# Kernel tuning notes

Measured on AMD Instinct MI355X. Metric: run time of the kernel, lower is better.

## Reference

```python
import jax, jax.numpy as jnp
import numpy as np

V, E, H, L = 32000, 512, 512, 2


def _cell(x, h, c, Wih, Whh, bih, bhh):
    # PyTorch LSTM cell, gate order i,f,g,o
    g = x @ Wih.T + bih + h @ Whh.T + bhh
    i, f, gg, o = jnp.split(g, 4, axis=-1)
    c = jax.nn.sigmoid(f) * c + jax.nn.sigmoid(i) * jnp.tanh(gg)
    h = jax.nn.sigmoid(o) * jnp.tanh(c)
    return h, c


def _run_layer(x, p):
    # x: [B, S, in], scan over time
    B = x.shape[0]
    h0 = jnp.zeros((B, H), x.dtype)

    def step(carry, xt):
        h, c = carry
        h, c = _cell(xt, h, c, *p)
        return (h, c), h

    (hT, cT), hs = jax.lax.scan(step, (h0, h0), jnp.swapaxes(x, 0, 1))
    return jnp.swapaxes(hs, 0, 1), hT, cT


def _forward(xs, ys, emb, enc_p, dec_p, attn_W, comb_W):
    # ---- Encoder (2-layer unidirectional LSTM) ----
    x = emb[xs]                      # [B, Senc, E]
    hs, cs = [], []
    for l in range(L):
        x, hT, cT = _run_layer(x, enc_p[l])
        hs.append(hT)
        cs.append(cT)
    enc_out = x                      # [B, Senc, H] (top layer)
    h = jnp.stack(hs)                # [L, B, H]
    c = jnp.stack(cs)
    neg = (1.0 - (xs > 0).astype(enc_out.dtype)) * 1e20  # [B, Senc]
    emb_out = jax.lax.stop_gradient(emb)  # shared output weight is detached

    # ---- Decoder: per-timestep pre-attention ('general') + LSTM ----
    def step(carry, yt):
        h, c = carry
        xe = emb[yt]                              # [B, E]
        hid = h[-1] @ attn_W.T                    # [B, H]
        pw = jnp.einsum('bh,bsh->bs', hid, enc_out) - neg
        aw = jax.nn.softmax(pw, axis=1)
        ctx = jnp.einsum('bs,bsh->bh', aw, enc_out)
        inp = jnp.tanh(jnp.concatenate([xe, ctx], axis=1) @ comb_W.T)  # [B, E]
        nh, nc = [], []
        for l in range(L):
            hl, cl = _cell(inp, h[l], c[l], *dec_p[l])
            nh.append(hl)
            nc.append(cl)
            inp = hl
        sc = inp @ emb_out.T                      # [B, V] (o2e is identity, e2s shared)
        return (jnp.stack(nh), jnp.stack(nc)), sc

    _, scores = jax.lax.scan(step, (h, c), jnp.swapaxes(ys, 0, 1))
    return jnp.swapaxes(scores, 0, 1)             # [B, Sdec, V]


def setup_inputs() -> dict:
    key = jax.random.key(0)
    B, Senc, Sdec = 32, 64, 32
    d = {}
    d['xs'] = jax.random.randint(jax.random.fold_in(key, 0), (B, Senc), 1, V)
    d['ys'] = jax.random.randint(jax.random.fold_in(key, 1), (B, Sdec), 1, V)
    d['emb'] = jax.random.normal(jax.random.fold_in(key, 2), (V, E), dtype=jnp.float32) * 0.02
    s = float(1.0 / np.sqrt(H))
    i = 3
    for pre in ('enc', 'dec'):
        for l in range(L):
            ind = E if l == 0 else H
            for name, shape in ((pre + '_Wih' + str(l), (4 * H, ind)),
                                (pre + '_Whh' + str(l), (4 * H, H)),
                                (pre + '_bih' + str(l), (4 * H,)),
                                (pre + '_bhh' + str(l), (4 * H,))):
                d[name] = jax.random.uniform(jax.random.fold_in(key, i), shape, minval=-s, maxval=s)
                i += 1
    d['attn_W'] = jax.random.uniform(jax.random.fold_in(key, i), (H, H), minval=-s, maxval=s)
    d['comb_W'] = jax.random.uniform(jax.random.fold_in(key, i + 1), (E, H + E), minval=-s, maxval=s)
    return d


def reference(xs, ys, emb,
              enc_Wih0, enc_Whh0, enc_bih0, enc_bhh0,
              enc_Wih1, enc_Whh1, enc_bih1, enc_bhh1,
              dec_Wih0, dec_Whh0, dec_bih0, dec_bhh0,
              dec_Wih1, dec_Whh1, dec_bih1, dec_bhh1,
              attn_W, comb_W):
    enc_p = [(enc_Wih0, enc_Whh0, enc_bih0, enc_bhh0),
             (enc_Wih1, enc_Whh1, enc_bih1, enc_bhh1)]
    dec_p = [(dec_Wih0, dec_Whh0, dec_bih0, dec_bhh0),
             (dec_Wih1, dec_Whh1, dec_bih1, dec_bhh1)]
    scores = _forward(xs, ys, emb, enc_p, dec_p, attn_W, comb_W)
    preds = jnp.argmax(scores[..., 1:], axis=-1) + 1   # skip padding idx 0
    return preds, scores
```

## Files before the change

### kernel.cpp

```cpp
#include <hip/hip_runtime.h>
#include <math.h>

#define B 32
#define SENC 64
#define SDEC 32
#define HDIM 512
#define EDIM 512
#define VDIM 32000
#define G4 2048
#define BH (B*HDIM)
#define NBLK 256

__device__ __forceinline__ void agent_st(float* p, float v)
{
    __hip_atomic_store(p, v, __ATOMIC_RELAXED, __HIP_MEMORY_SCOPE_AGENT);
}
__device__ __forceinline__ float4 agent_ld4(const float* p)
{
    float4 v;
    asm volatile("global_load_dwordx4 %0, %1, off sc0 sc1"
                 : "=v"(v) : "v"(p) : "memory");
    return v;
}

__device__ __forceinline__ void grid_barrier_h(unsigned* bar, int xcd, unsigned ep)
{
    asm volatile("s_waitcnt vmcnt(0) lgkmcnt(0)" ::: "memory");
    __syncthreads();
    if (threadIdx.x == 0) {
        unsigned* xcnt = bar + xcd * 16;
        unsigned* gcnt = bar + 256;
        unsigned* rfl  = bar + 512 + xcd * 16;
        unsigned prev = __hip_atomic_fetch_add(xcnt, 1u, __ATOMIC_RELAXED,
                                               __HIP_MEMORY_SCOPE_AGENT);
        if (prev == ep * 32u - 1u) {
            __hip_atomic_fetch_add(gcnt, 1u, __ATOMIC_RELAXED,
                                   __HIP_MEMORY_SCOPE_AGENT);
            while (__hip_atomic_load(gcnt, __ATOMIC_RELAXED,
                                     __HIP_MEMORY_SCOPE_AGENT) < ep * 8u)
                __builtin_amdgcn_s_sleep(1);
            __hip_atomic_store(rfl, ep, __ATOMIC_RELAXED,
                               __HIP_MEMORY_SCOPE_AGENT);
        } else {
            while (__hip_atomic_load(rfl, __ATOMIC_RELAXED,
                                     __HIP_MEMORY_SCOPE_AGENT) < ep)
                __builtin_amdgcn_s_sleep(2);
        }
        asm volatile("" ::: "memory");
    }
    __syncthreads();
}

__global__ __launch_bounds__(128) void embed_kernel(const int* __restrict__ toks,
                                                    const float* __restrict__ emb,
                                                    float* __restrict__ out)
{
    int t = blockIdx.x;
    int id = toks[t];
    const float4* src = (const float4*)(emb + (size_t)id * EDIM);
    float4* dst = (float4*)(out + (size_t)t * EDIM);
    dst[threadIdx.x] = src[threadIdx.x];
}

__global__ __launch_bounds__(256) void gemm_nt128(const float* __restrict__ A,
                                                  const float* __restrict__ Bm,
                                                  float* __restrict__ C,
                                                  const float* __restrict__ bias0,
                                                  const float* __restrict__ bias1,
                                                  int M, int N, int K, int ldb)
{
    __shared__ float As[16][128];
    __shared__ float Bs[16][128];
    int tid = threadIdx.x;
    int tx = tid & 15, ty = tid >> 4;
    int m0 = blockIdx.y * 128, n0 = blockIdx.x * 128;

    float acc[8][8];
    #pragma unroll
    for (int i = 0; i < 8; i++)
        #pragma unroll
        for (int j = 0; j < 8; j++) acc[i][j] = 0.f;

    int lr = tid >> 1, lk = (tid & 1) * 8;
    const float* Aptr = A + (size_t)(m0 + lr) * K + lk;
    const float* Bptr = Bm + (size_t)(n0 + lr) * ldb + lk;

    for (int k0 = 0; k0 < K; k0 += 16) {
        float4 a1 = *(const float4*)(Aptr + k0);
        float4 a2 = *(const float4*)(Aptr + k0 + 4);
        float4 b1 = *(const float4*)(Bptr + k0);
        float4 b2 = *(const float4*)(Bptr + k0 + 4);
        As[lk + 0][lr] = a1.x; As[lk + 1][lr] = a1.y;
        As[lk + 2][lr] = a1.z; As[lk + 3][lr] = a1.w;
        As[lk + 4][lr] = a2.x; As[lk + 5][lr] = a2.y;
        As[lk + 6][lr] = a2.z; As[lk + 7][lr] = a2.w;
        Bs[lk + 0][lr] = b1.x; Bs[lk + 1][lr] = b1.y;
        Bs[lk + 2][lr] = b1.z; Bs[lk + 3][lr] = b1.w;
        Bs[lk + 4][lr] = b2.x; Bs[lk + 5][lr] = b2.y;
        Bs[lk + 6][lr] = b2.z; Bs[lk + 7][lr] = b2.w;
        __syncthreads();
        #pragma unroll
        for (int kk = 0; kk < 16; kk++) {
            float4 av1 = *(const float4*)&As[kk][ty * 8];
            float4 av2 = *(const float4*)&As[kk][ty * 8 + 4];
            float4 bv1 = *(const float4*)&Bs[kk][tx * 8];
            float4 bv2 = *(const float4*)&Bs[kk][tx * 8 + 4];
            float am[8] = {av1.x, av1.y, av1.z, av1.w, av2.x, av2.y, av2.z, av2.w};
            float bn[8] = {bv1.x, bv1.y, bv1.z, bv1.w, bv2.x, bv2.y, bv2.z, bv2.w};
            #pragma unroll
            for (int i = 0; i < 8; i++)
                #pragma unroll
                for (int j = 0; j < 8; j++)
                    acc[i][j] += am[i] * bn[j];
        }
        __syncthreads();
    }

    int nc = n0 + tx * 8;
    float bb[8];
    #pragma unroll
    for (int j = 0; j < 8; j++) {
        bb[j] = 0.f;
        if (bias0) bb[j] += bias0[nc + j];
        if (bias1) bb[j] += bias1[nc + j];
    }
    #pragma unroll
    for (int i = 0; i < 8; i++) {
        int row = m0 + ty * 8 + i;
        float4 o1 = make_float4(acc[i][0] + bb[0], acc[i][1] + bb[1],
                                acc[i][2] + bb[2], acc[i][3] + bb[3]);
        float4 o2 = make_float4(acc[i][4] + bb[4], acc[i][5] + bb[5],
                                acc[i][6] + bb[6], acc[i][7] + bb[7]);
        *(float4*)(C + (size_t)row * N + nc) = o1;
        *(float4*)(C + (size_t)row * N + nc + 4) = o2;
    }
}

__global__ __launch_bounds__(256) void gemm_nn128(const float* __restrict__ A,
                                                  const float* __restrict__ Bm,
                                                  float* __restrict__ C,
                                                  int M, int N, int K)
{
    __shared__ float As[16][128];
    __shared__ float Bs[16][128];
    int tid = threadIdx.x;
    int tx = tid & 15, ty = tid >> 4;
    int m0 = blockIdx.y * 128, n0 = blockIdx.x * 128;

    float acc[8][8];
    #pragma unroll
    for (int i = 0; i < 8; i++)
        #pragma unroll
        for (int j = 0; j < 8; j++) acc[i][j] = 0.f;

    int lr = tid >> 1, lk = (tid & 1) * 8;
    const float* Aptr = A + (size_t)(m0 + lr) * K + lk;
    int bk = tid >> 5;
    int bn = (tid & 31) << 2;

    for (int k0 = 0; k0 < K; k0 += 16) {
        float4 a1 = *(const float4*)(Aptr + k0);
        float4 a2 = *(const float4*)(Aptr + k0 + 4);
        float4 v1 = *(const float4*)(Bm + (size_t)(k0 + bk) * N + n0 + bn);
        float4 v2 = *(const float4*)(Bm + (size_t)(k0 + bk + 8) * N + n0 + bn);
        As[lk + 0][lr] = a1.x; As[lk + 1][lr] = a1.y;
        As[lk + 2][lr] = a1.z; As[lk + 3][lr] = a1.w;
        As[lk + 4][lr] = a2.x; As[lk + 5][lr] = a2.y;
        As[lk + 6][lr] = a2.z; As[lk + 7][lr] = a2.w;
        *(float4*)&Bs[bk][bn] = v1;
        *(float4*)&Bs[bk + 8][bn] = v2;
        __syncthreads();
        #pragma unroll
        for (int kk = 0; kk < 16; kk++) {
            float4 av1 = *(const float4*)&As[kk][ty * 8];
            float4 av2 = *(const float4*)&As[kk][ty * 8 + 4];
            float4 bv1 = *(const float4*)&Bs[kk][tx * 8];
            float4 bv2 = *(const float4*)&Bs[kk][tx * 8 + 4];
            float am[8] = {av1.x, av1.y, av1.z, av1.w, av2.x, av2.y, av2.z, av2.w};
            float bv[8] = {bv1.x, bv1.y, bv1.z, bv1.w, bv2.x, bv2.y, bv2.z, bv2.w};
            #pragma unroll
            for (int i = 0; i < 8; i++)
                #pragma unroll
                for (int j = 0; j < 8; j++)
                    acc[i][j] += am[i] * bv[j];
        }
        __syncthreads();
    }

    int nc = n0 + tx * 8;
    #pragma unroll
    for (int i = 0; i < 8; i++) {
        int row = m0 + ty * 8 + i;
        float4 o1 = make_float4(acc[i][0], acc[i][1], acc[i][2], acc[i][3]);
        float4 o2 = make_float4(acc[i][4], acc[i][5], acc[i][6], acc[i][7]);
        *(float4*)(C + (size_t)row * N + nc) = o1;
        *(float4*)(C + (size_t)row * N + nc + 4) = o2;
    }
}

__device__ __forceinline__ float allreduce64(float v)
{
    #pragma unroll
    for (int m = 1; m < 64; m <<= 1) v += __shfl_xor(v, m);
    return v;
}

__device__ __forceinline__ float2 lstm_update(float i_, float f_, float g_,
                                              float o_, float c)
{
    float ig = 1.f / (1.f + expf(-i_));
    float fg = 1.f / (1.f + expf(-f_));
    float gg = tanhf(g_);
    float og = 1.f / (1.f + expf(-o_));
    float cn = fg * c + ig * gg;
    float hn = og * tanhf(cn);
    return make_float2(hn, cn);
}

__global__ __launch_bounds__(256) void enc_fused(
    const float* __restrict__ xg, const float* __restrict__ Whh0,
    const float* __restrict__ Wih1, const float* __restrict__ Whh1,
    const float* __restrict__ bih1, const float* __restrict__ bhh1,
    float* __restrict__ l1out, float* __restrict__ h0buf,
    float* __restrict__ h1buf, float* __restrict__ hT, float* __restrict__ cT,
    unsigned* __restrict__ bar)
{
    __shared__ __align__(16) float hs[16][520];
    __shared__ __align__(16) float is_[16][520];
    __shared__ float gacc[8][16][5];
    int blk = blockIdx.x;
    int xcd = blk & 7, slot = blk >> 3;
    int role = slot >> 4;
    int s2 = slot & 15;
    int jgroup = xcd * 8 + (s2 >> 1);
    int bg2 = s2 & 1;
    int tid = threadIdx.x;
    int r = tid >> 3, bb = tid & 7;
    int g = r >> 3, jj = r & 7;
    int row = (g << 9) + (jgroup << 3) + jj;
    int b0 = (bg2 << 4) + bb;
    const float* w0 = role ? (Wih1 + (size_t)row * 512)
                           : (Whh0 + (size_t)row * 512);
    const float* w1 = role ? (Whh1 + (size_t)row * 512) : (const float*)0;
    float bsum = role ? (bih1[row] + bhh1[row]) : 0.f;
    float creg = 0.f;
    unsigned ep = 0;
    int p = 0;
    for (int u = 0; u <= SENC; ++u) {
        int active = role ? (u >= 1) : (u < SENC);
        int t = role ? (u - 1) : u;
        if (active) {
            if (!role) {
                if (t == 0) {
                    float4 z = make_float4(0.f, 0.f, 0.f, 0.f);
                    #pragma unroll
                    for (int v = 0; v < 8; v++) {
                        int d = (tid + (v << 8)) << 2;
                        *(float4*)&hs[d >> 9][d & 511] = z;
                    }
                } else {
                    const float4* s4 = (const float4*)(h0buf + p * BH + ((bg2 << 4) << 9));
                    float4 hv[8];
                    #pragma unroll
                    for (int v = 0; v < 8; v++)
                        hv[v] = agent_ld4((const float*)(s4 + tid + (v << 8)));
                    asm volatile("s_waitcnt vmcnt(0)" ::: "memory");
                    #pragma unroll
                    for (int v = 0; v < 8; v++) {
                        int d = (tid + (v << 8)) << 2;
                        *(float4*)&hs[d >> 9][d & 511] = hv[v];
                    }
                }
            } else {
                const float4* s40 = (const float4*)(h0buf + p * BH + ((bg2 << 4) << 9));
                float4 hv[8];
                #pragma unroll
                for (int v = 0; v < 8; v++)
                    hv[v] = agent_ld4((const float*)(s40 + tid + (v << 8)));
                if (t == 0) {
                    asm volatile("s_waitcnt vmcnt(0)" ::: "memory");
                    float4 z = make_float4(0.f, 0.f, 0.f, 0.f);
                    #pragma unroll
                    for (int v = 0; v < 8; v++) {
                        int d = (tid + (v << 8)) << 2;
                        *(float4*)&hs[d >> 9][d & 511] = hv[v];
                        *(float4*)&is_[d >> 9][d & 511] = z;
                    }
                } else {
                    const float4* s41 = (const float4*)(h1buf + p * BH + ((bg2 << 4) << 9));
                    float4 iv[8];
                    #pragma unroll
                    for (int v = 0; v < 8; v++)
                        iv[v] = agent_ld4((const float*)(s41 + tid + (v << 8)));
                    asm volatile("s_waitcnt vmcnt(0)" ::: "memory");
                    #pragma unroll
                    for (int v = 0; v < 8; v++) {
                        int d = (tid + (v << 8)) << 2;
                        *(float4*)&hs[d >> 9][d & 511] = hv[v];
                        *(float4*)&is_[d >> 9][d & 511] = iv[v];
                    }
                }
            }
            __syncthreads();
            float acc0, acc1;
            if (!role) {
                acc0 = xg[(size_t)(b0 * SENC + t) * G4 + row];
                acc1 = xg[(size_t)((b0 + 8) * SENC + t) * G4 + row];
                float a00 = 0, a01 = 0, a02 = 0, a03 = 0;
                float a10 = 0, a11 = 0, a12 = 0, a13 = 0;
                const float* ha = hs[bb];
                const float* hb = hs[bb + 8];
                #pragma unroll 4
                for (int k = 0; k < 512; k += 4) {
                    float4 w = *(const float4*)(w0 + k);
                    float4 x = *(const float4*)(ha + k);
                    float4 y = *(const float4*)(hb + k);
                    a00 += w.x * x.x; a01 += w.y * x.y;
                    a02 += w.z * x.z; a03 += w.w * x.w;
                    a10 += w.x * y.x; a11 += w.y * y.y;
                    a12 += w.z * y.z; a13 += w.w * y.w;
                }
                acc0 += (a00 + a01) + (a02 + a03);
                acc1 += (a10 + a11) + (a12 + a13);
            } else {
                float a00 = 0, a01 = 0, a02 = 0, a03 = 0;
                float a10 = 0, a11 = 0, a12 = 0, a13 = 0;
                const float* h0a = hs[bb];
                const float* h0b = hs[bb + 8];
                const float* h1a = is_[bb];
                const float* h1b = is_[bb + 8];
                #pragma unroll 2
                for (int k = 0; k < 512; k += 4) {
                    float4 wi = *(const float4*)(w0 + k);
                    float4 wh = *(const float4*)(w1 + k);
                    float4 xa = *(const float4*)(h0a + k);
                    float4 xb = *(const float4*)(h0b + k);
                    float4 ya = *(const float4*)(h1a + k);
                    float4 yb = *(const float4*)(h1b + k);
                    a00 += wi.x * xa.x + wh.x * ya.x;
                    a01 += wi.y * xa.y + wh.y * ya.y;
                    a02 += wi.z * xa.z + wh.z * ya.z;
                    a03 += wi.w * xa.w + wh.w * ya.w;
                    a10 += wi.x * xb.x + wh.x * yb.x;
                    a11 += wi.y * xb.y + wh.y * yb.y;
                    a12 += wi.z * xb.z + wh.z * yb.z;
                    a13 += wi.w * xb.w + wh.w * yb.w;
                }
                acc0 = bsum + (a00 + a01) + (a02 + a03);
                acc1 = bsum + (a10 + a11) + (a12 + a13);
            }
            gacc[jj][bb][g] = acc0;
            gacc[jj][bb + 8][g] = acc1;
            __syncthreads();
            if (tid < 128) {
                int ujj = tid & 7, ulb = tid >> 3;
                float g0 = gacc[ujj][ulb][0], g1 = gacc[ujj][ulb][1];
                float g2 = gacc[ujj][ulb][2], g3 = gacc[ujj][ulb][3];
                float2 hc = lstm_update(g0, g1, g2, g3, creg);
                creg = hc.y;
                int ub = (bg2 << 4) + ulb;
                int ujh = (jgroup << 3) + ujj;
                if (!role) {
                    agent_st(h0buf + (p ^ 1) * BH + ub * 512 + ujh, hc.x);
                    if (t == SENC - 1) {
                        hT[ub * 512 + ujh] = hc.x;
                        cT[ub * 512 + ujh] = hc.y;
                    }
                } else {
                    agent_st(h1buf + (p ^ 1) * BH + ub * 512 + ujh, hc.x);
                    l1out[(size_t)(ub * SENC + t) * 512 + ujh] = hc.x;
                    if (t == SENC - 1) {
                        hT[BH + ub * 512 + ujh] = hc.x;
                        cT[BH + ub * 512 + ujh] = hc.y;
                    }
                }
            }
        }
        ep++;
        grid_barrier_h(bar, xcd, ep);
        p ^= 1;
    }
}

__device__ __forceinline__ void cell_phase(
    const float* __restrict__ Wih, const float* __restrict__ Whh,
    float bsum,
    const float* __restrict__ inp, const float* __restrict__ h_in,
    float* __restrict__ h_out, float* __restrict__ seqout,
    float& creg, int t, int jg, int bg, int row,
    float (*hs)[520], float (*is_)[520], float (*gacc)[8][5])
{
    int tid = threadIdx.x;
    {
        const float4* hsrc4 = (const float4*)(h_in + ((bg << 3) << 9));
        const float4* isrc4 = (const float4*)(inp + ((bg << 3) << 9));
        float4 hv4[4], iv4[4];
        #pragma unroll
        for (int u = 0; u < 4; u++) {
            hv4[u] = agent_ld4((const float*)(hsrc4 + tid + (u << 8)));
            iv4[u] = agent_ld4((const float*)(isrc4 + tid + (u << 8)));
        }
        asm volatile("s_waitcnt vmcnt(0)" ::: "memory");
        #pragma unroll
        for (int u = 0; u < 4; u++) {
            int d = (tid + (u << 8)) << 2;
            int rb = d >> 9, kk = d & 511;
            *(float4*)&hs[rb][kk] = hv4[u];
            *(float4*)&is_[rb][kk] = iv4[u];
        }
    }
    __syncthreads();
    int r = tid >> 3, bb = tid & 7;
    int g = r >> 3, jj = r & 7;
    const float* wi = Wih + (size_t)row * 512;
    const float* wh = Whh + (size_t)row * 512;
    const float* ir = is_[bb];
    const float* hr = hs[bb];
    float a0 = 0.f, a1 = 0.f, a2 = 0.f, a3 = 0.f;
    #pragma unroll 8
    for (int k = 0; k < 512; k += 4) {
        float4 wiv = *(const float4*)(wi + k);
        float4 iv = *(const float4*)(ir + k);
        float4 whv = *(const float4*)(wh + k);
        float4 hv = *(const float4*)(hr + k);
        a0 += wiv.x * iv.x + whv.x * hv.x;
        a1 += wiv.y * iv.y + whv.y * hv.y;
        a2 += wiv.z * iv.z + whv.z * hv.z;
        a3 += wiv.w * iv.w + whv.w * hv.w;
    }
    gacc[jj][bb][g] = bsum + (a0 + a1) + (a2 + a3);
    __syncthreads();
    if (tid < 64) {
        int ujj = tid & 7, ubb = tid >> 3;
        float g0 = gacc[ujj][ubb][0], g1 = gacc[ujj][ubb][1];
        float g2 = gacc[ujj][ubb][2], g3 = gacc[ujj][ubb][3];
        float2 hc = lstm_update(g0, g1, g2, g3, creg);
        creg = hc.y;
        int ub = (bg << 3) + ubb, ujh = (jg << 3) + ujj;
        agent_st(h_out + ub * 512 + ujh, hc.x);
        if (seqout) seqout[(size_t)(ub * SDEC + t) * 512 + ujh] = hc.x;
    }
}

__global__ __launch_bounds__(256) void decoder_persist(
    const int* __restrict__ xs,
    const float* __restrict__ enc_out, const float* __restrict__ encT,
    const float* __restrict__ yg, const float* __restrict__ comb_W,
    const float* __restrict__ Wih0, const float* __restrict__ Whh0,
    const float* __restrict__ bih0, const float* __restrict__ bhh0,
    const float* __restrict__ Wih1, const float* __restrict__ Whh1,
    const float* __restrict__ bih1, const float* __restrict__ bhh1,
    const float* __restrict__ hT0, const float* __restrict__ cT0,
    const float* __restrict__ hT1, const float* __restrict__ cT1,
    float* __restrict__ dhb0, float* __restrict__ dhb1,
    float* __restrict__ inpbuf, float* __restrict__ h2seq,
    unsigned* __restrict__ bar)
{
    __shared__ __align__(16) float hs[8][520];
    __shared__ __align__(16) float is_[8][520];
    __shared__ float gacc[8][8][5];
    __shared__ __align__(16) float h2s[512];
    __shared__ __align__(16) float ctxs[512];
    __shared__ float pw[64];
    __shared__ float aw[64];
    int blk = blockIdx.x;
    int xcd = blk & 7, slot = blk >> 3;
    int jg = xcd * 8 + (slot >> 2), bg = slot & 3;
    int ab = xcd * 4 + (slot >> 3);
    int e0 = (slot & 7) << 6;
    int tid = threadIdx.x;
    int lane = tid & 63, wv = tid >> 6;
    int r = tid >> 3;
    int g = r >> 3, jj = r & 7;
    int row = (g << 9) + (jg << 3) + jj;
    float bsum0 = bih0[row] + bhh0[row];
    float bsum1 = bih1[row] + bhh1[row];
    float c0 = 0.f, c1 = 0.f;
    if (tid < 64) {
        int ujj = tid & 7, ubb = tid >> 3;
        int ub = (bg << 3) + ubb, ujh = (jg << 3) + ujj;
        c0 = cT0[ub * 512 + ujh];
        c1 = cT1[ub * 512 + ujh];
    }
    unsigned ep = 0;
    int p = 0;
    for (int t = 0; t < SDEC; ++t) {
        int q = p ^ 1;
        {
            const float* h2p = ((t == 0) ? hT1 : dhb1 + p * BH) + ab * 512;
            if (tid < 128) {
                float4 v = agent_ld4((const float*)((const float4*)h2p + tid));
                asm volatile("s_waitcnt vmcnt(0)" ::: "memory");
                ((float4*)h2s)[tid] = v;
            }
            __syncthreads();
            for (int s = wv; s < SENC; s += 4) {
                const float* rowp = encT + (size_t)(ab * SENC + s) * 512;
                float pp = 0.f;
                #pragma unroll
                for (int i = 0; i < 8; i++)
                    pp += h2s[lane + 64 * i] * rowp[lane + 64 * i];
                pp = allreduce64(pp);
                if (lane == 0)
                    pw[s] = pp - ((xs[ab * SENC + s] > 0) ? 0.f : 1e20f);
            }
            __syncthreads();
            if (tid < 64) {
                float v = pw[tid];
                float m = v;
                #pragma unroll
                for (int o = 1; o < 64; o <<= 1) m = fmaxf(m, __shfl_xor(m, o));
                float ex = expf(v - m);
                float sm = ex;
                #pragma unroll
                for (int o = 1; o < 64; o <<= 1) sm += __shfl_xor(sm, o);
                aw[tid] = ex / sm;
            }
            __syncthreads();
            for (int e = tid; e < 512; e += 256) {
                float s0 = 0.f, s1 = 0.f, s2 = 0.f, s3 = 0.f;
                #pragma unroll
                for (int ss = 0; ss < SENC; ss += 4) {
                    s0 += aw[ss + 0] * enc_out[(size_t)(ab * SENC + ss + 0) * 512 + e];
                    s1 += aw[ss + 1] * enc_out[(size_t)(ab * SENC + ss + 1) * 512 + e];
                    s2 += aw[ss + 2] * enc_out[(size_t)(ab * SENC + ss + 2) * 512 + e];
                    s3 += aw[ss + 3] * enc_out[(size_t)(ab * SENC + ss + 3) * 512 + e];
                }
                ctxs[e] = (s0 + s1) + (s2 + s3);
            }
            __syncthreads();
            for (int e = wv; e < 64; e += 4) {
                const float* rowp = comb_W + (size_t)(e0 + e) * 1024 + 512;
                float pp = 0.f;
                #pragma unroll
                for (int i = 0; i < 8; i++)
                    pp += ctxs[lane + 64 * i] * rowp[lane + 64 * i];
                pp = allreduce64(pp);
                if (lane == 0)
                    agent_st(inpbuf + ab * 512 + e0 + e,
                             tanhf(yg[(size_t)(ab * SDEC + t) * 512 + e0 + e] + pp));
            }
        }
        ep++; grid_barrier_h(bar, xcd, ep);
        cell_phase(Wih0, Whh0, bsum0, inpbuf,
                   (t == 0) ? hT0 : dhb0 + p * BH, dhb0 + q * BH,
                   (float*)nullptr, c0, t, jg, bg, row, hs, is_, gacc);
        ep++; grid_barrier_h(bar, xcd, ep);
        cell_phase(Wih1, Whh1, bsum1, dhb0 + q * BH,
                   (t == 0) ? hT1 : dhb1 + p * BH, dhb1 + q * BH,
                   h2seq, c1, t, jg, bg, row, hs, is_, gacc);
        ep++; grid_barrier_h(bar, xcd, ep);
        p = q;
    }
}

__global__ __launch_bounds__(256) void argmax_kernel(const float* __restrict__ scores,
                                                     float* __restrict__ preds)
{
    __shared__ float sv[256];
    __shared__ int si[256];
    int m = blockIdx.x;
    const float* row = scores + (size_t)m * VDIM;
    float best = -3.4e38f;
    int bi = 0x7fffffff;
    for (int v = 1 + (int)threadIdx.x; v < VDIM; v += 256) {
        float val = row[v];
        if (val > best) { best = val; bi = v; }
    }
    sv[threadIdx.x] = best;
    si[threadIdx.x] = bi;
    __syncthreads();
    for (int s = 128; s > 0; s >>= 1) {
        if ((int)threadIdx.x < s) {
            float ov = sv[threadIdx.x + s];
            int oi = si[threadIdx.x + s];
            if (ov > sv[threadIdx.x] ||
                (ov == sv[threadIdx.x] && oi < si[threadIdx.x])) {
                sv[threadIdx.x] = ov;
                si[threadIdx.x] = oi;
            }
        }
        __syncthreads();
    }
    if (threadIdx.x == 0) preds[m] = (float)si[0];
}

extern "C" void kernel_launch(void* const* d_in, const int* in_sizes, int n_in,
                              void* d_out, int out_size, void* d_ws, size_t ws_size,
                              hipStream_t stream)
{
    const int* xs = (const int*)d_in[0];
    const int* ys = (const int*)d_in[1];
    const float* emb = (const float*)d_in[2];
    const float* W[16];
    for (int i = 0; i < 16; i++) W[i] = (const float*)d_in[3 + i];
    const float* attn_W = (const float*)d_in[19];
    const float* comb_W = (const float*)d_in[20];
    float* out = (float*)d_out;
    float* ws = (float*)d_ws;

    float* xemb   = ws;
    float* xg     = xemb + 1048576;
    float* l1out  = xg + 4194304;
    float* encT   = l1out + 1048576;
    float* h0buf  = encT + 1048576;
    float* h1buf  = h0buf + 2 * BH;
    float* hT     = h1buf + 2 * BH;
    float* cT     = hT + 2 * BH;
    unsigned* barcnt = (unsigned*)(cT + 2 * BH);
    float* yemb   = xemb;
    float* h2seq  = xg;
    float* inpbuf = xg + 524288;
    float* dhb0   = inpbuf + BH;
    float* dhb1   = dhb0 + 2 * BH;
    float* yg     = dhb1 + 2 * BH;

    hipMemsetAsync(barcnt, 0, 2 * 4096, stream);

    embed_kernel<<<B * SENC, 128, 0, stream>>>(xs, emb, xemb);
    gemm_nt128<<<dim3(G4 / 128, (B * SENC) / 128), 256, 0, stream>>>(
        xemb, W[0], xg, W[2], W[3], B * SENC, G4, 512, 512);
    embed_kernel<<<B * SDEC, 128, 0, stream>>>(ys, emb, yemb);
    {
        const float* xgp = xg;
        const float* whh0 = W[1];
        const float* wih1 = W[4];
        const float* whh1 = W[5];
        const float* bih1 = W[6];
        const float* bhh1 = W[7];
        float* l1o = l1out;
        float* h0b = h0buf;
        float* h1b = h1buf;
        float* hTp = hT;
        float* cTp = cT;
        unsigned* bp = barcnt;
        void* eargs[] = {(void*)&xgp, (void*)&whh0, (void*)&wih1, (void*)&whh1,
                         (void*)&bih1, (void*)&bhh1, (void*)&l1o, (void*)&h0b,
                         (void*)&h1b, (void*)&hTp, (void*)&cTp, (void*)&bp};
        hipLaunchCooperativeKernel((void*)enc_fused, dim3(NBLK), dim3(256),
                                   eargs, 0, stream);
    }

    gemm_nn128<<<dim3(512 / 128, (B * SENC) / 128), 256, 0, stream>>>(
        l1out, attn_W, encT, B * SENC, 512, 512);
    gemm_nt128<<<dim3(512 / 128, (B * SDEC) / 128), 256, 0, stream>>>(
        yemb, comb_W, yg, nullptr, nullptr, B * SDEC, 512, 512, 1024);

    {
        const int* xs_ = xs;
        const float* enc_out_ = l1out;
        const float* encT_ = encT;
        const float* yg_ = yg;
        const float* combW_ = comb_W;
        const float* wih0 = W[8];
        const float* whh0 = W[9];
        const float* bih0 = W[10];
        const float* bhh0 = W[11];
        const float* wih1 = W[12];
        const float* whh1 = W[13];
        const float* bih1 = W[14];
        const float* bhh1 = W[15];
        const float* hT0_ = hT;
        const float* cT0_ = cT;
        const float* hT1_ = hT + BH;
        const float* cT1_ = cT + BH;
        float* dhb0_ = dhb0;
        float* dhb1_ = dhb1;
        float* inp_ = inpbuf;
        float* h2seq_ = h2seq;
        unsigned* bp = barcnt + 1024;
        void* dargs[] = {(void*)&xs_, (void*)&enc_out_, (void*)&encT_,
                         (void*)&yg_, (void*)&combW_,
                         (void*)&wih0, (void*)&whh0, (void*)&bih0, (void*)&bhh0,
                         (void*)&wih1, (void*)&whh1, (void*)&bih1, (void*)&bhh1,
                         (void*)&hT0_, (void*)&cT0_, (void*)&hT1_, (void*)&cT1_,
                         (void*)&dhb0_, (void*)&dhb1_, (void*)&inp_, (void*)&h2seq_,
                         (void*)&bp};
        hipLaunchCooperativeKernel((void*)decoder_persist, dim3(NBLK), dim3(256),
                                   dargs, 0, stream);
    }

    gemm_nt128<<<dim3(VDIM / 128, (B * SDEC) / 128), 256, 0, stream>>>(
        h2seq, emb, out + B * SDEC, nullptr, nullptr, B * SDEC, VDIM, 512, 512);
    argmax_kernel<<<B * SDEC, 256, 0, stream>>>(out + B * SDEC, out);
}
```

Measured before the change: 3.623 ms.

## Precompute encoder outputs projected by comb_W context half before decoder loop

Uses linearity: ctx @ Wc^T = aw @ (enc_out @ Wc^T), so a one-off GEMM computes encC = enc_out @ comb_W[:,512:]^T before the decoder. Each decoder block then needs only a 64-wide weighted sum over encC for its slice instead of the full 512-wide context plus a 64x512 matvec against comb_W every timestep. This removes per-step redundant context computation across blocks and a sync phase, at the cost of an extra GEMM and workspace buffer.

Measured after the change: 3.369 ms. 1.08x faster.

```diff
diff --git a/kernel.cpp b/kernel.cpp
--- a/kernel.cpp
+++ b/kernel.cpp
@@ -444,8 +444,8 @@
 
 __global__ __launch_bounds__(256) void decoder_persist(
     const int* __restrict__ xs,
-    const float* __restrict__ enc_out, const float* __restrict__ encT,
-    const float* __restrict__ yg, const float* __restrict__ comb_W,
+    const float* __restrict__ encT, const float* __restrict__ encC,
+    const float* __restrict__ yg,
     const float* __restrict__ Wih0, const float* __restrict__ Whh0,
     const float* __restrict__ bih0, const float* __restrict__ bhh0,
     const float* __restrict__ Wih1, const float* __restrict__ Whh1,
@@ -460,7 +460,7 @@
     __shared__ __align__(16) float is_[8][520];
     __shared__ float gacc[8][8][5];
     __shared__ __align__(16) float h2s[512];
-    __shared__ __align__(16) float ctxs[512];
+    __shared__ float psum[4][64];
     __shared__ float pw[64];
     __shared__ float aw[64];
     int blk = blockIdx.x;
@@ -517,28 +517,20 @@
                 aw[tid] = ex / sm;
             }
             __syncthreads();
-            for (int e = tid; e < 512; e += 256) {
-                float s0 = 0.f, s1 = 0.f, s2 = 0.f, s3 = 0.f;
+            {
+                float part = 0.f;
+                const float* cb = encC + (size_t)(ab * SENC + (wv << 4)) * 512
+                                + e0 + lane;
                 #pragma unroll
-                for (int ss = 0; ss < SENC; ss += 4) {
-                    s0 += aw[ss + 0] * enc_out[(size_t)(ab * SENC + ss + 0) * 512 + e];
-                    s1 += aw[ss + 1] * enc_out[(size_t)(ab * SENC + ss + 1) * 512 + e];
-                    s2 += aw[ss + 2] * enc_out[(size_t)(ab * SENC + ss + 2) * 512 + e];
-                    s3 += aw[ss + 3] * enc_out[(size_t)(ab * SENC + ss + 3) * 512 + e];
-                }
-                ctxs[e] = (s0 + s1) + (s2 + s3);
+                for (int si = 0; si < 16; si++)
+                    part += aw[(wv << 4) + si] * cb[si * 512];
+                psum[wv][lane] = part;
             }
             __syncthreads();
-            for (int e = wv; e < 64; e += 4) {
-                const float* rowp = comb_W + (size_t)(e0 + e) * 1024 + 512;
-                float pp = 0.f;
-                #pragma unroll
-                for (int i = 0; i < 8; i++)
-                    pp += ctxs[lane + 64 * i] * rowp[lane + 64 * i];
-                pp = allreduce64(pp);
-                if (lane == 0)
-                    agent_st(inpbuf + ab * 512 + e0 + e,
-                             tanhf(yg[(size_t)(ab * SDEC + t) * 512 + e0 + e] + pp));
+            if (tid < 64) {
+                float v = psum[0][tid] + psum[1][tid] + psum[2][tid] + psum[3][tid];
+                float rr = tanhf(yg[(size_t)(ab * SDEC + t) * 512 + e0 + tid] + v);
+                agent_st(inpbuf + ab * 512 + e0 + tid, rr);
             }
         }
         ep++; grid_barrier_h(bar, xcd, ep);
@@ -614,6 +606,7 @@
     float* dhb0   = inpbuf + BH;
     float* dhb1   = dhb0 + 2 * BH;
     float* yg     = dhb1 + 2 * BH;
+    float* encC   = yg + 524288;
 
     hipMemsetAsync(barcnt, 0, 2 * 4096, stream);
 
@@ -645,13 +638,14 @@
         l1out, attn_W, encT, B * SENC, 512, 512);
     gemm_nt128<<<dim3(512 / 128, (B * SDEC) / 128), 256, 0, stream>>>(
         yemb, comb_W, yg, nullptr, nullptr, B * SDEC, 512, 512, 1024);
+    gemm_nt128<<<dim3(512 / 128, (B * SENC) / 128), 256, 0, stream>>>(
+        l1out, comb_W + 512, encC, nullptr, nullptr, B * SENC, 512, 512, 1024);
 
     {
         const int* xs_ = xs;
-        const float* enc_out_ = l1out;
         const float* encT_ = encT;
+        const float* encC_ = encC;
         const float* yg_ = yg;
-        const float* combW_ = comb_W;
         const float* wih0 = W[8];
         const float* whh0 = W[9];
         const float* bih0 = W[10];
@@ -669,8 +663,8 @@
         float* inp_ = inpbuf;
         float* h2seq_ = h2seq;
         unsigned* bp = barcnt + 1024;
-        void* dargs[] = {(void*)&xs_, (void*)&enc_out_, (void*)&encT_,
-                         (void*)&yg_, (void*)&combW_,
+        void* dargs[] = {(void*)&xs_, (void*)&encT_, (void*)&encC_,
+                         (void*)&yg_,
                          (void*)&wih0, (void*)&whh0, (void*)&bih0, (void*)&bhh0,
                          (void*)&wih1, (void*)&whh1, (void*)&bih1, (void*)&bhh1,
                          (void*)&hT0_, (void*)&cT0_, (void*)&hT1_, (void*)&cT1_,
```
